# Kernel optimization log

Measured on AMD Instinct MI355X. Metric: run time of the kernel, lower is better.

## Reference

```python
import jax, jax.numpy as jnp
import numpy as np

B, L, D, NHEADS, P = 64, 256, 768, 8, 3
VOCAB, DEP, NLAYERS = 30522, 45, 2
LAM = 0.5


def _forward(src_mask, aspect_mask, lex, attention_mask,
             tok_emb, seg_emb, pool_w, pool_b, ln_a, ln_b,
             dep_emb, fc1_w, fc1_b, fc2_w, fc2_b,
             aq_w, aq_b, ak_w, ak_b, lq_w, lq_b, lk_w, lk_b, root_w,
             gcn_w, gcn_b, fc3_w, fc3_b, cls_w, cls_b, vlin_w,
             text_bert_indices, bert_segments_ids, ori_tag, head):
    b, l = text_bert_indices.shape
    d = tok_emb.shape[1]
    dk = d // NHEADS
    NEG = jnp.float32(-1e30)
    # stand-in BERT encoder: token + segment embeddings, tanh pooler on [CLS]
    seq = tok_emb[text_bert_indices] + seg_emb[bert_segments_ids]
    pooled = jnp.tanh(seq[:, 0] @ pool_w + pool_b)
    # torch LayerNorm variant: unbiased std (ddof=1)
    mean = seq.mean(-1, keepdims=True)
    std = jnp.std(seq, axis=-1, keepdims=True, ddof=1)
    gcn_in = ln_a * (seq - mean) / (std + 1e-6) + ln_b
    # in-place fmask[:,0]=1 mutates src_mask storage in torch -> effective mask
    sm = src_mask.at[:, 0].set(1.0)
    # dependency-tag score -> per-token softmax -> scatter into [L,L] adjacency
    dep_h = jax.nn.relu(dep_emb[ori_tag] @ fc1_w + fc1_b)
    dep_s = (dep_h @ fc2_w + fc2_b)[..., 0]                      # [B,L]
    dep_feat = jax.nn.softmax(dep_s * sm + (1.0 - sm) * NEG, axis=1)
    to_idx = jnp.arange(1, l)
    fro = head[:, :l - 1]                                        # [B,L-1]
    b_idx = jnp.arange(b)[:, None]
    vals = dep_feat[:, :l - 1]
    dep_adj = jnp.ones((b, l, l), jnp.float32)
    dep_adj = dep_adj.at[b_idx, fro, to_idx[None, :]].set(vals)
    dep_adj = dep_adj.at[b_idx, to_idx[None, :], fro].set(vals)
    # multi-head attention-as-adjacency (returns softmax weights only)
    q = (gcn_in @ aq_w + aq_b).reshape(b, l, NHEADS, dk).transpose(0, 2, 1, 3)
    k = (gcn_in @ ak_w + ak_b).reshape(b, l, NHEADS, dk).transpose(0, 2, 1, 3)
    scores = jnp.einsum('bhqd,bhkd->bhqk', q, k) / (jnp.sqrt(jnp.float32(dk)) + 1e-9)
    scores = jnp.where(sm[:, None, None, :] == 0, jnp.float32(-1e9), scores)
    adj_ag = jax.nn.softmax(scores, axis=-1).mean(axis=1)        # [B,L,L]
    eye = jnp.eye(l, dtype=jnp.float32)
    adj_ag = (adj_ag * (1.0 - eye) + eye) * sm[:, :, None]
    # structured latent attention (stand-in for missing StructuredAtt):
    # masked bilinear attention biased by dep_adj + root attention loss
    q2 = gcn_in @ lq_w + lq_b
    k2 = gcn_in @ lk_w + lk_b
    lat = jnp.einsum('bqd,bkd->bqk', q2, k2) / jnp.sqrt(jnp.float32(d))
    lat = lat + dep_adj + (1.0 - sm)[:, None, :] * (-10000.0)
    adj_latent = jax.nn.softmax(lat, axis=-1)
    root_p = jax.nn.softmax((gcn_in @ root_w)[..., 0] * sm + (1.0 - sm) * NEG, axis=1)
    loss_root = -jnp.mean(jnp.log(jnp.sum(root_p * aspect_mask, axis=1) + 1e-9))
    adj_latent = (adj_latent * (1.0 - eye) + eye) * sm[:, :, None]
    # gated dual-adjacency GCN layers
    H_l = gcn_in
    I_sem = gcn_in
    for layer in range(gcn_w.shape[0]):
        g_l = jax.nn.sigmoid(H_l)
        I_sem = (adj_ag @ H_l) @ gcn_w[layer] + gcn_b[layer]
        I_lat = (adj_latent @ H_l) @ gcn_w[layer] + gcn_b[layer]
        g = jax.nn.sigmoid(I_lat)
        lam_g = LAM * g
        I_com = (1.0 - lam_g) * I_sem + lam_g * I_lat
        H_out = jax.nn.relu(I_com @ fc3_w + fc3_b)
        H_l = g_l * H_out + (1.0 - g_l) * H_l
    # readout
    asp_wn = aspect_mask.sum(axis=1, keepdims=True)              # [B,1]
    m3 = sm[:, :, None]
    h_l = H_l * m3
    h_sem = I_sem * m3
    beta = jnp.einsum('bqd,bkd->bqk', h_l, h_sem) / 1000.0
    attn_o = jax.nn.softmax(beta.sum(axis=1, keepdims=True), axis=2)  # [B,1,L]
    outputs = (attn_o @ I_sem)[:, 0]                             # [B,D]
    sem_pool = (I_sem * aspect_mask[:, :, None]).sum(axis=1) / (asp_wn + 1e-9)
    final = jnp.concatenate([outputs, sem_pool, pooled], axis=-1)  # [B,3D]
    logits = final @ cls_w + cls_b
    e = (H_l @ vlin_w)[..., 0]
    lw = jax.nn.softmax(e, axis=1) * 50.0
    lw = lw * sm.at[:, 0].set(0.0)
    lexicon_loss = jnp.mean((lw - lex) ** 2)
    return logits, loss_root, lexicon_loss


def setup_inputs() -> dict:
    key = jax.random.key(0)
    ks = jax.random.split(key, 24)
    s = 0.02
    n = lambda i, shape: jax.random.normal(ks[i], shape, dtype=jnp.float32) * s
    inp = {}
    inp['text_bert_indices'] = jax.random.randint(ks[0], (B, L), 0, VOCAB, dtype=jnp.int32)
    inp['bert_segments_ids'] = jnp.zeros((B, L), jnp.int32)
    inp['attention_mask'] = jnp.ones((B, L), jnp.float32)
    inp['src_mask'] = jnp.ones((B, L), jnp.float32)
    inp['aspect_mask'] = jax.random.randint(ks[1], (B, L), 0, 2).astype(jnp.float32)
    inp['lex'] = jax.random.uniform(ks[2], (B, L), dtype=jnp.float32)
    inp['ori_tag'] = jax.random.randint(ks[3], (B, L), 0, DEP, dtype=jnp.int32)
    inp['head'] = jax.random.randint(ks[4], (B, L), 0, L, dtype=jnp.int32)
    inp['tok_emb'] = n(5, (VOCAB, D)); inp['seg_emb'] = n(6, (2, D))
    inp['pool_w'] = n(7, (D, D)); inp['pool_b'] = jnp.zeros((D,), jnp.float32)
    inp['ln_a'] = jnp.ones((D,), jnp.float32); inp['ln_b'] = jnp.zeros((D,), jnp.float32)
    inp['dep_emb'] = n(8, (DEP, 300))
    inp['fc1_w'] = n(9, (300, 256)); inp['fc1_b'] = jnp.zeros((256,), jnp.float32)
    inp['fc2_w'] = n(10, (256, 1)); inp['fc2_b'] = jnp.zeros((1,), jnp.float32)
    inp['aq_w'] = n(11, (D, D)); inp['aq_b'] = jnp.zeros((D,), jnp.float32)
    inp['ak_w'] = n(12, (D, D)); inp['ak_b'] = jnp.zeros((D,), jnp.float32)
    inp['lq_w'] = n(13, (D, D)); inp['lq_b'] = jnp.zeros((D,), jnp.float32)
    inp['lk_w'] = n(14, (D, D)); inp['lk_b'] = jnp.zeros((D,), jnp.float32)
    inp['root_w'] = n(15, (D, 1))
    inp['gcn_w'] = n(16, (NLAYERS, D, D)); inp['gcn_b'] = jnp.zeros((NLAYERS, D), jnp.float32)
    inp['fc3_w'] = n(17, (D, D)); inp['fc3_b'] = jnp.zeros((D,), jnp.float32)
    inp['cls_w'] = n(18, (3 * D, P)); inp['cls_b'] = jnp.zeros((P,), jnp.float32)
    inp['vlin_w'] = n(19, (D, 1))
    return inp


def reference(text_bert_indices, bert_segments_ids, attention_mask, src_mask, aspect_mask, lex,
              ori_tag, head, tok_emb, seg_emb, pool_w, pool_b, ln_a, ln_b, dep_emb,
              fc1_w, fc1_b, fc2_w, fc2_b, aq_w, aq_b, ak_w, ak_b, lq_w, lq_b, lk_w, lk_b,
              root_w, gcn_w, gcn_b, fc3_w, fc3_b, cls_w, cls_b, vlin_w):
    return _forward(src_mask, aspect_mask, lex, attention_mask,
                    tok_emb, seg_emb, pool_w, pool_b, ln_a, ln_b,
                    dep_emb, fc1_w, fc1_b, fc2_w, fc2_b,
                    aq_w, aq_b, ak_w, ak_b, lq_w, lq_b, lk_w, lk_b, root_w,
                    gcn_w, gcn_b, fc3_w, fc3_b, cls_w, cls_b, vlin_w,
                    text_bert_indices, bert_segments_ids, ori_tag, head)
```

## Files before the change

kernel.cpp:

```cpp
#include <hip/hip_runtime.h>
#include <hip/hip_bf16.h>
#include <math.h>

#define DI __device__ __forceinline__

constexpr int cB = 64, cL = 256, cD = 768;
constexpr long BLD = (long)cB * cL * cD;
constexpr long BLL = (long)cB * cL * cL;
constexpr long cLL = (long)cL * cL;
constexpr long cLD = (long)cL * cD;

typedef __attribute__((ext_vector_type(8))) short b8;
typedef __attribute__((ext_vector_type(4))) float f4;

#define GLDS(g, l)                                                    \
  __builtin_amdgcn_global_load_lds(                                   \
      (const __attribute__((address_space(1))) void*)(g),             \
      (__attribute__((address_space(3))) void*)(l), 16, 0, 0)

DI float wsum(float v) {
#pragma unroll
  for (int o = 32; o > 0; o >>= 1) v += __shfl_down(v, o, 64);
  return v;
}
DI float wsum_all(float v) {
#pragma unroll
  for (int m = 32; m > 0; m >>= 1) v += __shfl_xor(v, m, 64);
  return v;
}
DI float wmaxr(float v) {
#pragma unroll
  for (int o = 32; o > 0; o >>= 1) v = fmaxf(v, __shfl_down(v, o, 64));
  return v;
}
DI float blockSum(float v) {
  __shared__ float sh[4];
  v = wsum(v);
  __syncthreads();
  if ((threadIdx.x & 63) == 0) sh[threadIdx.x >> 6] = v;
  __syncthreads();
  return sh[0] + sh[1] + sh[2] + sh[3];
}
DI float blockMax(float v) {
  __shared__ float sh[4];
  v = wmaxr(v);
  __syncthreads();
  if ((threadIdx.x & 63) == 0) sh[threadIdx.x >> 6] = v;
  __syncthreads();
  return fmaxf(fmaxf(sh[0], sh[1]), fmaxf(sh[2], sh[3]));
}
DI float sigf(float x) { return 1.f / (1.f + expf(-x)); }

template <int OBF, int RELU, int BIAS, int EPI, int SWZ>
__global__ __launch_bounds__(256, 2) void bgemm(
    const __hip_bfloat16* __restrict__ A, const __hip_bfloat16* __restrict__ BT,
    void* __restrict__ Cv, const float* __restrict__ bias,
    float* __restrict__ auxf, __hip_bfloat16* __restrict__ auxb,
    int K, int lda, int ldb, int ldc,
    int zshift, int zmask, long sA1, long sA2, long sB1, long sB2, long sC,
    int czdiv) {
  __shared__ __hip_bfloat16 Asp[128 * 32];
  __shared__ __hip_bfloat16 Bsp[128 * 32];
  int bx = blockIdx.x, by = blockIdx.y;
  if (SWZ) {
    int gx = gridDim.x;
    int nb = gx * gridDim.y;
    int id = by * gx + bx;
    int cpx = nb >> 3;
    id = (id & 7) * cpx + (id >> 3);
    bx = id % gx;
    by = id / gx;
  }
  int z = blockIdx.z;
  A += (long)(z >> zshift) * sA1 + (long)(z & zmask) * sA2;
  BT += (long)(z >> zshift) * sB1 + (long)(z & zmask) * sB2;
  int tid = threadIdx.x;
  int lane = tid & 63, w = tid >> 6;
  int wr = w >> 1, wc = w & 1;
  int l16 = lane & 15, q = lane >> 4;
  int m0 = by << 7, n0 = bx << 7;

  int fm = tid >> 2, fq = tid & 3;
  const __hip_bfloat16* Ap0 = A + (long)(m0 + fm) * lda + fq * 8;
  const __hip_bfloat16* Ap1 = A + (long)(m0 + fm + 64) * lda + fq * 8;
  const __hip_bfloat16* Bp0 = BT + (long)(n0 + fm) * ldb + fq * 8;
  const __hip_bfloat16* Bp1 = BT + (long)(n0 + fm + 64) * ldb + fq * 8;
  char* Aw0 = (char*)Asp + (w << 10);
  char* Aw1 = (char*)Asp + 4096 + (w << 10);
  char* Bw0 = (char*)Bsp + (w << 10);
  char* Bw1 = (char*)Bsp + 4096 + (w << 10);

  f4 acc[4][4];
#pragma unroll
  for (int i = 0; i < 4; i++)
#pragma unroll
    for (int j = 0; j < 4; j++) acc[i][j] = (f4){0.f, 0.f, 0.f, 0.f};

  for (int k0 = 0; k0 < K; k0 += 32) {
    GLDS(Ap0 + k0, Aw0);
    GLDS(Ap1 + k0, Aw1);
    GLDS(Bp0 + k0, Bw0);
    GLDS(Bp1 + k0, Bw1);
    __syncthreads();
    b8 af[4], bf[4];
#pragma unroll
    for (int i = 0; i < 4; i++)
      af[i] = *(const b8*)&Asp[(wr * 64 + i * 16 + l16) * 32 + q * 8];
#pragma unroll
    for (int j = 0; j < 4; j++)
      bf[j] = *(const b8*)&Bsp[(wc * 64 + j * 16 + l16) * 32 + q * 8];
#pragma unroll
    for (int i = 0; i < 4; i++)
#pragma unroll
      for (int j = 0; j < 4; j++)
        acc[i][j] = __builtin_amdgcn_mfma_f32_16x16x32_bf16(af[i], bf[j], acc[i][j], 0, 0, 0);
    __syncthreads();
  }
  if (EPI == 4) {
#pragma unroll
    for (int j = 0; j < 4; j++) {
      int n = n0 + wc * 64 + j * 16 + l16;
#pragma unroll
      for (int i = 0; i < 4; i++) {
        int m = m0 + wr * 64 + i * 16 + (q << 2);
        __hip_bfloat16 t4[4];
#pragma unroll
        for (int r = 0; r < 4; r++) t4[r] = __float2bfloat16(acc[i][j][r]);
        long bidx = (long)(m >> 8) * sC + (long)n * cL + (m & 255);
        *(uint2*)&((__hip_bfloat16*)Cv)[bidx] = *(uint2*)t4;
      }
    }
    return;
  }
  long cz = (long)(z >> czdiv) * sC;
#pragma unroll
  for (int j = 0; j < 4; j++) {
    int n = n0 + wc * 64 + j * 16 + l16;
    float bv = BIAS ? bias[n] : 0.f;
#pragma unroll
    for (int i = 0; i < 4; i++) {
#pragma unroll
      for (int r = 0; r < 4; r++) {
        int m = m0 + wr * 64 + i * 16 + q * 4 + r;
        long idx = cz + (long)m * ldc + n;
        float v = acc[i][j][r] + bv;
        if (EPI == 0) {
          if (RELU) v = fmaxf(v, 0.f);
          if (OBF)
            ((__hip_bfloat16*)Cv)[idx] = __float2bfloat16(v);
          else
            ((float*)Cv)[idx] = v;
        } else {
          v = fmaxf(v, 0.f);
          float h = __bfloat162float(auxb[idx]);
          float g = sigf(h);
          float o = h + g * (v - h);
          auxb[idx] = __float2bfloat16(o);
          if (auxf) auxf[idx] = o;
        }
      }
    }
  }
}

__global__ __launch_bounds__(256, 2) void bgemm_dual(
    const __hip_bfloat16* __restrict__ A1g, const __hip_bfloat16* __restrict__ A2g,
    const __hip_bfloat16* __restrict__ BTg, float* __restrict__ IsemF,
    __hip_bfloat16* __restrict__ Icb, const float* __restrict__ bias,
    int write_isem) {
  __shared__ __hip_bfloat16 A1sp[128 * 32];
  __shared__ __hip_bfloat16 A2sp[128 * 32];
  __shared__ __hip_bfloat16 Bsp[128 * 32];
  int id = (blockIdx.z * 2 + blockIdx.y) * 6 + blockIdx.x;
  id = (id & 7) * 96 + (id >> 3);
  int bx = id % 6, t = id / 6;
  int by = t & 1, z = t >> 1;
  const __hip_bfloat16* A1 = A1g + (long)z * cLL;
  const __hip_bfloat16* A2 = A2g + (long)z * cLL;
  const __hip_bfloat16* BT = BTg + (long)z * cLD;
  int tid = threadIdx.x;
  int lane = tid & 63, w = tid >> 6;
  int wr = w >> 1, wc = w & 1;
  int l16 = lane & 15, q = lane >> 4;
  int m0 = by << 7, n0 = bx << 7;

  int fm = tid >> 2, fq = tid & 3;
  const __hip_bfloat16* A1p0 = A1 + (long)(m0 + fm) * cL + fq * 8;
  const __hip_bfloat16* A1p1 = A1p0 + 64L * cL;
  const __hip_bfloat16* A2p0 = A2 + (long)(m0 + fm) * cL + fq * 8;
  const __hip_bfloat16* A2p1 = A2p0 + 64L * cL;
  const __hip_bfloat16* Bp0 = BT + (long)(n0 + fm) * cL + fq * 8;
  const __hip_bfloat16* Bp1 = Bp0 + 64L * cL;
  char* w10 = (char*)A1sp + (w << 10);
  char* w11 = (char*)A1sp + 4096 + (w << 10);
  char* w20 = (char*)A2sp + (w << 10);
  char* w21 = (char*)A2sp + 4096 + (w << 10);
  char* wb0 = (char*)Bsp + (w << 10);
  char* wb1 = (char*)Bsp + 4096 + (w << 10);

  f4 ac1[4][4], ac2[4][4];
#pragma unroll
  for (int i = 0; i < 4; i++)
#pragma unroll
    for (int j = 0; j < 4; j++) {
      ac1[i][j] = (f4){0.f, 0.f, 0.f, 0.f};
      ac2[i][j] = (f4){0.f, 0.f, 0.f, 0.f};
    }

  for (int k0 = 0; k0 < cL; k0 += 32) {
    GLDS(A1p0 + k0, w10);
    GLDS(A1p1 + k0, w11);
    GLDS(A2p0 + k0, w20);
    GLDS(A2p1 + k0, w21);
    GLDS(Bp0 + k0, wb0);
    GLDS(Bp1 + k0, wb1);
    __syncthreads();
    b8 a1f[4], a2f[4], bf[4];
#pragma unroll
    for (int i = 0; i < 4; i++) {
      a1f[i] = *(const b8*)&A1sp[(wr * 64 + i * 16 + l16) * 32 + q * 8];
      a2f[i] = *(const b8*)&A2sp[(wr * 64 + i * 16 + l16) * 32 + q * 8];
    }
#pragma unroll
    for (int j = 0; j < 4; j++)
      bf[j] = *(const b8*)&Bsp[(wc * 64 + j * 16 + l16) * 32 + q * 8];
#pragma unroll
    for (int i = 0; i < 4; i++)
#pragma unroll
      for (int j = 0; j < 4; j++) {
        ac1[i][j] = __builtin_amdgcn_mfma_f32_16x16x32_bf16(a1f[i], bf[j], ac1[i][j], 0, 0, 0);
        ac2[i][j] = __builtin_amdgcn_mfma_f32_16x16x32_bf16(a2f[i], bf[j], ac2[i][j], 0, 0, 0);
      }
    __syncthreads();
  }
  long cz = (long)z * cLD;
#pragma unroll
  for (int j = 0; j < 4; j++) {
    int n = n0 + wc * 64 + j * 16 + l16;
    float bv = bias[n];
#pragma unroll
    for (int i = 0; i < 4; i++) {
#pragma unroll
      for (int r = 0; r < 4; r++) {
        int m = m0 + wr * 64 + i * 16 + q * 4 + r;
        long idx = cz + (long)m * cD + n;
        float is = ac1[i][j][r] + bv;
        float il = ac2[i][j][r] + bv;
        float g = 0.5f * sigf(il);
        Icb[idx] = __float2bfloat16(is + g * (il - is));
        if (write_isem) IsemF[idx] = is;
      }
    }
  }
}

__global__ __launch_bounds__(256, 2) void k_qkadj2(
    const __hip_bfloat16* __restrict__ qkb, const float* __restrict__ src_mask,
    const int* __restrict__ headv, const float* __restrict__ df,
    __hip_bfloat16* __restrict__ outAag, __hip_bfloat16* __restrict__ outAlat) {
  const bool lat = blockIdx.z != 0;
  const int NH = lat ? 1 : 8;
  const int KH = lat ? 768 : 96;
  const int QOFF = lat ? 1536 : 0;
  const int KOFF = lat ? 2304 : 768;
  const float scale = lat ? (1.f / sqrtf(768.f)) : (1.f / (sqrtf(96.f) + 1e-9f));
  __shared__ __hip_bfloat16 Qs[64 * 32];
  __shared__ __hip_bfloat16 Ks[256 * 32];
  __shared__ float red[4][64];
  const int b = blockIdx.y, m0 = blockIdx.x << 6;
  const int tid = threadIdx.x, lane = tid & 63, w = tid >> 6;
  const int l16 = lane & 15, q = lane >> 4;
  const long rowbase = (long)b * cL;
  const __hip_bfloat16* Qg = qkb + (rowbase + m0 + (tid >> 2)) * 3072 + (tid & 3) * 8 + QOFF;
  const __hip_bfloat16* Kg = qkb + (rowbase + (tid >> 2)) * 3072 + (tid & 3) * 8 + KOFF;
  char* qdst = (char*)Qs + (w << 10);

  float smj[4];
  int hcol[4];
  float dfc[4];
#pragma unroll
  for (int j = 0; j < 4; j++) {
    int col = w * 64 + j * 16 + l16;
    smj[j] = (col == 0) ? 1.f : src_mask[b * cL + col];
    if (lat) {
      hcol[j] = (col >= 1) ? headv[b * cL + col - 1] : -1;
      dfc[j] = (col >= 1) ? df[b * cL + col - 1] : 0.f;
    }
  }
  float smi_[4][4];
  int hrow_[4][4];
  float dfr_[4][4];
#pragma unroll
  for (int i = 0; i < 4; i++)
#pragma unroll
    for (int r = 0; r < 4; r++) {
      int grow = m0 + i * 16 + q * 4 + r;
      smi_[i][r] = (grow == 0) ? 1.f : src_mask[b * cL + grow];
      if (lat) {
        hrow_[i][r] = (grow >= 1) ? headv[b * cL + grow - 1] : -1;
        dfr_[i][r] = (grow >= 1) ? df[b * cL + grow - 1] : 0.f;
      }
    }

  f4 aag[4][4];
#pragma unroll
  for (int i = 0; i < 4; i++)
#pragma unroll
    for (int j = 0; j < 4; j++) aag[i][j] = (f4){0.f, 0.f, 0.f, 0.f};

  f4 sa[4][4];
  float inv_[4][4];
  for (int h = 0; h < NH; h++) {
    const int hk = h * 96;
#pragma unroll
    for (int i = 0; i < 4; i++)
#pragma unroll
      for (int j = 0; j < 4; j++) sa[i][j] = (f4){0.f, 0.f, 0.f, 0.f};
    for (int k0 = 0; k0 < KH; k0 += 32) {
      __syncthreads();
      GLDS(Qg + hk + k0, qdst);
#pragma unroll
      for (int u = 0; u < 4; u++)
        GLDS(Kg + (long)u * 196608 + hk + k0, (char*)Ks + u * 4096 + (w << 10));
      __syncthreads();
      b8 af[4], bf[4];
#pragma unroll
      for (int i = 0; i < 4; i++)
        af[i] = *(const b8*)&Qs[(i * 16 + l16) * 32 + q * 8];
#pragma unroll
      for (int j = 0; j < 4; j++)
        bf[j] = *(const b8*)&Ks[(w * 64 + j * 16 + l16) * 32 + q * 8];
#pragma unroll
      for (int i = 0; i < 4; i++)
#pragma unroll
        for (int j = 0; j < 4; j++)
          sa[i][j] = __builtin_amdgcn_mfma_f32_16x16x32_bf16(af[i], bf[j], sa[i][j], 0, 0, 0);
    }
#pragma unroll
    for (int i = 0; i < 4; i++)
#pragma unroll
      for (int j = 0; j < 4; j++)
#pragma unroll
        for (int r = 0; r < 4; r++) {
          float raw = sa[i][j][r];
          float v;
          if (lat) {
            int grow = m0 + i * 16 + q * 4 + r;
            int col = w * 64 + j * 16 + l16;
            float dep = 1.f;
            if (hcol[j] == grow) dep = dfc[j];
            if (col == hrow_[i][r]) dep = dfr_[i][r];
            v = raw * scale + dep + (1.f - smj[j]) * -10000.f;
          } else {
            v = (smj[j] == 0.f) ? -1e9f : raw * scale;
          }
          sa[i][j][r] = v;
        }
    float rm_[4][4];
#pragma unroll
    for (int i = 0; i < 4; i++)
#pragma unroll
      for (int r = 0; r < 4; r++) {
        float m = fmaxf(fmaxf(sa[i][0][r], sa[i][1][r]), fmaxf(sa[i][2][r], sa[i][3][r]));
#pragma unroll
        for (int o = 1; o < 16; o <<= 1) m = fmaxf(m, __shfl_xor(m, o, 64));
        if (l16 == 0) red[w][i * 16 + q * 4 + r] = m;
        rm_[i][r] = m;
      }
    __syncthreads();
#pragma unroll
    for (int i = 0; i < 4; i++)
#pragma unroll
      for (int r = 0; r < 4; r++) {
        int lr = i * 16 + q * 4 + r;
        rm_[i][r] = fmaxf(fmaxf(red[0][lr], red[1][lr]), fmaxf(red[2][lr], red[3][lr]));
      }
    __syncthreads();
#pragma unroll
    for (int i = 0; i < 4; i++)
#pragma unroll
      for (int r = 0; r < 4; r++) {
        float s0 = 0.f;
#pragma unroll
        for (int j = 0; j < 4; j++) {
          float e = expf(sa[i][j][r] - rm_[i][r]);
          sa[i][j][r] = e;
          s0 += e;
        }
#pragma unroll
        for (int o = 1; o < 16; o <<= 1) s0 += __shfl_xor(s0, o, 64);
        if (l16 == 0) red[w][i * 16 + q * 4 + r] = s0;
      }
    __syncthreads();
#pragma unroll
    for (int i = 0; i < 4; i++)
#pragma unroll
      for (int r = 0; r < 4; r++) {
        int lr = i * 16 + q * 4 + r;
        inv_[i][r] = 1.f / (red[0][lr] + red[1][lr] + red[2][lr] + red[3][lr]);
      }
    if (!lat) {
#pragma unroll
      for (int i = 0; i < 4; i++)
#pragma unroll
        for (int j = 0; j < 4; j++)
#pragma unroll
          for (int r = 0; r < 4; r++) aag[i][j][r] += sa[i][j][r] * inv_[i][r];
    }
  }
  __hip_bfloat16* outA = lat ? outAlat : outAag;
#pragma unroll
  for (int j = 0; j < 4; j++) {
    int col = w * 64 + j * 16 + l16;
#pragma unroll
    for (int i = 0; i < 4; i++)
#pragma unroll
      for (int r = 0; r < 4; r++) {
        int grow = m0 + i * 16 + q * 4 + r;
        float p = lat ? sa[i][j][r] * inv_[i][r] : aag[i][j][r] * 0.125f;
        float v = (col == grow) ? 1.f : p;
        outA[((long)b * cL + grow) * cL + col] = __float2bfloat16(v * smi_[i][r]);
      }
  }
}

__global__ void k_wconv7(const float* __restrict__ s0, const float* __restrict__ s1,
                         const float* __restrict__ s2, const float* __restrict__ s3,
                         const float* __restrict__ s4, const float* __restrict__ s5,
                         const float* __restrict__ s6, __hip_bfloat16* __restrict__ dst,
                         const float* __restrict__ ba, const float* __restrict__ bb,
                         const float* __restrict__ bc, const float* __restrict__ bd,
                         float* __restrict__ catb) {
  if (blockIdx.z == 7) {
    if (blockIdx.y != 0 || blockIdx.x >= 12) return;
    int tid = threadIdx.y * 32 + threadIdx.x;
    int i = blockIdx.x * 256 + tid;
    float v = (i < 768) ? ba[i] : (i < 1536) ? bb[i - 768]
              : (i < 2304) ? bc[i - 1536] : bd[i - 2304];
    catb[i] = v;
    return;
  }
  const float* srcs[7] = {s0, s1, s2, s3, s4, s5, s6};
  const float* src = srcs[blockIdx.z];
  __hip_bfloat16* d = dst + (long)blockIdx.z * cD * cD;
  __shared__ float t[32][33];
  int k0 = blockIdx.x * 32, n0 = blockIdx.y * 32;
  int tx = threadIdx.x, ty = threadIdx.y;
#pragma unroll
  for (int i = 0; i < 32; i += 8) t[ty + i][tx] = src[(long)(k0 + ty + i) * cD + n0 + tx];
  __syncthreads();
#pragma unroll
  for (int i = 0; i < 32; i += 8)
    d[(long)(n0 + ty + i) * cD + k0 + tx] = __float2bfloat16(t[tx][ty + i]);
}

__global__ __launch_bounds__(256) void k_gcnin(
    const int* __restrict__ tbi, const int* __restrict__ bsi,
    const float* __restrict__ tok, const float* __restrict__ seg,
    const float* __restrict__ ln_a, const float* __restrict__ ln_b,
    const float* __restrict__ root_w, __hip_bfloat16* __restrict__ gib,
    float* __restrict__ x64, float* __restrict__ e1) {
  int wave = threadIdx.x >> 6, lane = threadIdx.x & 63;
  long bl = (long)blockIdx.x * 4 + wave;
  int t = tbi[bl], s = bsi[bl];
  const float* tr = tok + (long)t * cD;
  const float* sr = seg + (long)s * cD;
  float x[12];
  float ls = 0.f;
#pragma unroll
  for (int c = 0; c < 12; c++) {
    int d = lane + (c << 6);
    x[c] = tr[d] + sr[d];
    ls += x[c];
  }
  if ((bl & 255) == 0) {
#pragma unroll
    for (int c = 0; c < 12; c++) x64[(bl >> 8) * cD + lane + (c << 6)] = x[c];
  }
  float mean = wsum_all(ls) * (1.f / 768.f);
  float lv = 0.f;
#pragma unroll
  for (int c = 0; c < 12; c++) { float d2 = x[c] - mean; lv += d2 * d2; }
  float var = wsum_all(lv) * (1.f / 767.f);
  float inv = 1.f / (sqrtf(var) + 1e-6f);
  float rdot = 0.f;
#pragma unroll
  for (int c = 0; c < 12; c++) {
    int d = lane + (c << 6);
    float v = ln_a[d] * (x[c] - mean) * inv + ln_b[d];
    gib[bl * cD + d] = __float2bfloat16(v);
    rdot += v * root_w[d];
  }
  float tot = wsum_all(rdot);
  if (lane == 0) e1[bl] = tot;
}

__global__ __launch_bounds__(256) void k_pool1(
    const float* __restrict__ x64, const float* __restrict__ pw,
    float* __restrict__ pacc) {
  __shared__ float pws[48][256];
  __shared__ float xs[16][48];
  int i0 = blockIdx.x * 48, j0 = blockIdx.y * 256, b0 = blockIdx.z * 16;
  for (int r = 0; r < 48; r++) pws[r][threadIdx.x] = pw[(long)(i0 + r) * cD + j0 + threadIdx.x];
  for (int idx = threadIdx.x; idx < 16 * 48; idx += 256)
    xs[idx / 48][idx % 48] = x64[(long)(b0 + idx / 48) * cD + i0 + idx % 48];
  __syncthreads();
  int j = threadIdx.x;
  for (int b = 0; b < 16; b++) {
    float acc = 0.f;
#pragma unroll 8
    for (int i = 0; i < 48; i++) acc += xs[b][i] * pws[i][j];
    atomicAdd(&pacc[(long)(b0 + b) * cD + j0 + j], acc);
  }
}

__global__ __launch_bounds__(256) void k_s45(
    const float* __restrict__ dep_emb, const float* __restrict__ fc1w,
    const float* __restrict__ fc1b, const float* __restrict__ fc2w,
    const float* __restrict__ fc2b, float* __restrict__ s45) {
  int t = blockIdx.x;
  __shared__ float e[300];
  for (int i = threadIdx.x; i < 300; i += 256) e[i] = dep_emb[t * 300 + i];
  __syncthreads();
  int j = threadIdx.x;
  float h = fc1b[j];
  for (int i = 0; i < 300; i++) h += e[i] * fc1w[i * 256 + j];
  h = fmaxf(h, 0.f);
  float tot = blockSum(h * fc2w[j]);
  if (threadIdx.x == 0) s45[t] = tot + fc2b[0];
}

__global__ __launch_bounds__(256) void k_depfeat(
    const int* __restrict__ ori, const float* __restrict__ src_mask,
    const float* __restrict__ s45, float* __restrict__ dep_feat) {
  int b = blockIdx.x, l = threadIdx.x;
  float smv = (l == 0) ? 1.f : src_mask[b * cL + l];
  float sc = s45[ori[b * cL + l]] * smv + (1.f - smv) * (-1e30f);
  float mx = blockMax(sc);
  float ex = expf(sc - mx);
  float sum = blockSum(ex);
  dep_feat[b * cL + l] = ex / sum;
}

__global__ __launch_bounds__(256) void k_rowdot2(
    const float* __restrict__ Isem, const float* __restrict__ hlsum,
    const float* __restrict__ gcnH, const float* __restrict__ vlin,
    float* __restrict__ sraw, float* __restrict__ e2) {
  int r = blockIdx.x * 4 + (threadIdx.x >> 6);
  int lane = threadIdx.x & 63;
  bool z = blockIdx.y != 0;
  const float4* row = (const float4*)((z ? gcnH : Isem) + (long)r * cD);
  const float4* wp = z ? (const float4*)vlin
                       : (const float4*)(hlsum + (long)(r >> 8) * cD);
  float s = 0.f;
#pragma unroll
  for (int c = 0; c < 3; c++) {
    int idx = c * 64 + lane;
    float4 a = row[idx], b = wp[idx];
    s += a.x * b.x + a.y * b.y + a.z * b.z + a.w * b.w;
  }
  s = wsum(s);
  if (lane == 0) (z ? e2 : sraw)[r] = s;
}

__global__ __launch_bounds__(256) void k_tailred(
    const float* __restrict__ sraw, const float* __restrict__ e1,
    const float* __restrict__ e2, const float* __restrict__ src_mask,
    const float* __restrict__ aspect_mask, const float* __restrict__ lex,
    float* __restrict__ wgt, float* __restrict__ asum,
    float* __restrict__ out_root, float* __restrict__ out_lex) {
  int b = blockIdx.x, l = threadIdx.x;
  float smv = (l == 0) ? 1.f : src_mask[b * cL + l];
  float am = aspect_mask[b * cL + l];
  float s = sraw[b * cL + l] * smv * 0.001f;
  float mx = blockMax(s);
  float ex = expf(s - mx);
  float sum = blockSum(ex);
  wgt[b * cL + l] = ex / sum;
  float a = blockSum(am);
  if (l == 0) asum[b] = a;
  float sc = e1[b * cL + l] * smv + (1.f - smv) * (-1e30f);
  float mx2 = blockMax(sc);
  float ex2 = expf(sc - mx2);
  float sum2 = blockSum(ex2);
  float tot = blockSum((ex2 / sum2) * am);
  if (l == 0) atomicAdd(out_root, -logf(tot + 1e-9f) * (1.f / 64.f));
  float e = e2[b * cL + l];
  float mx3 = blockMax(e);
  float ex3 = expf(e - mx3);
  float sum3 = blockSum(ex3);
  float mult = (l == 0) ? 0.f : src_mask[b * cL + l];
  float lw = ex3 / sum3 * 50.f * mult;
  float d2 = lw - lex[b * cL + l];
  float t3 = blockSum(d2 * d2);
  if (l == 0) atomicAdd(out_lex, t3 * (1.f / (64.f * 256.f)));
}

__global__ __launch_bounds__(256) void k_hl(
    const float* __restrict__ H, const float* __restrict__ src_mask,
    float* __restrict__ hlsum) {
  int b = blockIdx.z, d = (blockIdx.y << 8) + threadIdx.x, l0 = blockIdx.x * 32;
  float acc = 0.f;
  for (int l = l0; l < l0 + 32; l++) {
    float smv = (l == 0) ? 1.f : src_mask[b * cL + l];
    acc += H[((long)b * cL + l) * cD + d] * smv;
  }
  atomicAdd(&hlsum[(long)b * cD + d], acc);
}

__global__ __launch_bounds__(256) void k_wsum(
    const float* __restrict__ Isem, const float* __restrict__ wgt,
    const float* __restrict__ am, float* __restrict__ outputs,
    float* __restrict__ sempool) {
  int b = blockIdx.z, d = (blockIdx.y << 8) + threadIdx.x, l0 = blockIdx.x * 32;
  float accO = 0.f, accS = 0.f;
  for (int l = l0; l < l0 + 32; l++) {
    float v = Isem[((long)b * cL + l) * cD + d];
    accO += wgt[b * cL + l] * v;
    accS += am[b * cL + l] * v;
  }
  atomicAdd(&outputs[(long)b * cD + d], accO);
  atomicAdd(&sempool[(long)b * cD + d], accS);
}

__global__ __launch_bounds__(256) void k_logits(
    const float* __restrict__ outputs, const float* __restrict__ sempool,
    const float* __restrict__ pacc, const float* __restrict__ pb,
    const float* __restrict__ asum, const float* __restrict__ cw,
    const float* __restrict__ cb, float* __restrict__ out) {
  int b = blockIdx.x;
  float inv = 1.f / (asum[b] + 1e-9f);
  float a0 = 0.f, a1 = 0.f, a2 = 0.f;
  for (int i = threadIdx.x; i < 3 * cD; i += 256) {
    float f;
    if (i < cD)
      f = outputs[(long)b * cD + i];
    else if (i < 2 * cD)
      f = sempool[(long)b * cD + i - cD] * inv;
    else
      f = tanhf(pacc[(long)b * cD + i - 2 * cD] + pb[i - 2 * cD]);
    a0 += f * cw[i * 3 + 0];
    a1 += f * cw[i * 3 + 1];
    a2 += f * cw[i * 3 + 2];
  }
  a0 = blockSum(a0);
  a1 = blockSum(a1);
  a2 = blockSum(a2);
  if (threadIdx.x == 0) {
    out[b * 3 + 0] = a0 + cb[0];
    out[b * 3 + 1] = a1 + cb[1];
    out[b * 3 + 2] = a2 + cb[2];
  }
}

extern "C" void kernel_launch(void* const* d_in, const int* in_sizes, int n_in,
                              void* d_out, int out_size, void* d_ws, size_t ws_size,
                              hipStream_t stream) {
  const int* tbi = (const int*)d_in[0];
  const int* bsi = (const int*)d_in[1];
  const float* src_mask = (const float*)d_in[3];
  const float* aspect_mask = (const float*)d_in[4];
  const float* lex = (const float*)d_in[5];
  const int* ori = (const int*)d_in[6];
  const int* head = (const int*)d_in[7];
  const float* tok_emb = (const float*)d_in[8];
  const float* seg_emb = (const float*)d_in[9];
  const float* pool_w = (const float*)d_in[10];
  const float* pool_b = (const float*)d_in[11];
  const float* ln_a = (const float*)d_in[12];
  const float* ln_b = (const float*)d_in[13];
  const float* dep_emb = (const float*)d_in[14];
  const float* fc1_w = (const float*)d_in[15];
  const float* fc1_b = (const float*)d_in[16];
  const float* fc2_w = (const float*)d_in[17];
  const float* fc2_b = (const float*)d_in[18];
  const float* aq_w = (const float*)d_in[19];
  const float* aq_b = (const float*)d_in[20];
  const float* ak_w = (const float*)d_in[21];
  const float* ak_b = (const float*)d_in[22];
  const float* lq_w = (const float*)d_in[23];
  const float* lq_b = (const float*)d_in[24];
  const float* lk_w = (const float*)d_in[25];
  const float* lk_b = (const float*)d_in[26];
  const float* root_w = (const float*)d_in[27];
  const float* gcn_w = (const float*)d_in[28];
  const float* gcn_b = (const float*)d_in[29];
  const float* fc3_w = (const float*)d_in[30];
  const float* fc3_b = (const float*)d_in[31];
  const float* cls_w = (const float*)d_in[32];
  const float* cls_b = (const float*)d_in[33];
  const float* vlin_w = (const float*)d_in[34];

  float* out = (float*)d_out;
  float* ws = (float*)d_ws;
  float* gcnH = ws;
  float* Isem = gcnH + BLD;
  float* depfeat = Isem + BLD;
  float* s45 = depfeat + cB * cL;
  float* pooled = s45 + 64;
  float* x64 = pooled + cB * cD;
  float* hlsum = x64 + cB * cD;
  float* outputs = hlsum + cB * cD;
  float* sempool = outputs + cB * cD;
  float* pacc = sempool + cB * cD;
  float* e1 = pacc + cB * cD;
  float* e2 = e1 + cB * cL;
  float* sraw = e2 + cB * cL;
  float* wgt = sraw + cB * cL;
  float* asum = wgt + cB * cL;
  float* catb = asum + 64;
  __hip_bfloat16* gib = (__hip_bfloat16*)(catb + 3072);
  __hip_bfloat16* qkb = gib + BLD;
  __hip_bfloat16* scores = qkb + 4 * BLD;
  __hip_bfloat16* adjag_b = scores + 8 * BLL;
  __hip_bfloat16* adjlat_b = adjag_b + BLL;
  __hip_bfloat16* wbt = adjlat_b + BLL;
  __hip_bfloat16* HWbT = qkb + BLD;
  __hip_bfloat16* Icb = qkb + 2 * BLD;

  hipMemsetAsync((char*)d_out + 192 * sizeof(float), 0, 2 * sizeof(float), stream);
  hipMemsetAsync(hlsum, 0, 4 * cB * cD * sizeof(float), stream);

  k_gcnin<<<cB * cL / 4, 256, 0, stream>>>(tbi, bsi, tok_emb, seg_emb, ln_a, ln_b,
                                           root_w, gib, x64, e1);
  k_s45<<<45, 256, 0, stream>>>(dep_emb, fc1_w, fc1_b, fc2_w, fc2_b, s45);
  k_depfeat<<<cB, 256, 0, stream>>>(ori, src_mask, s45, depfeat);
  k_pool1<<<dim3(16, 3, 4), 256, 0, stream>>>(x64, pool_w, pacc);
  k_wconv7<<<dim3(24, 24, 8), dim3(32, 8), 0, stream>>>(
      aq_w, ak_w, lq_w, lk_w, gcn_w, gcn_w + (long)cD * cD, fc3_w, wbt,
      aq_b, ak_b, lq_b, lk_b, catb);

  const long DD = (long)cD * cD;
  const long LD = cLD;

  bgemm<1, 0, 1, 0, 1><<<dim3(24, 128, 1), 256, 0, stream>>>(
      gib, wbt, qkb, catb, nullptr, nullptr, cD, cD, cD, 3072,
      0, 0, 0, 0, 0, 0, 0, 0);

  k_qkadj2<<<dim3(4, cB, 2), 256, 0, stream>>>(qkb, src_mask, head, depfeat,
                                               adjag_b, adjlat_b);

  for (int layer = 0; layer < 2; layer++) {
    const float* bb = gcn_b + (long)layer * cD;
    bgemm<1, 0, 0, 4, 1><<<dim3(6, 128, 1), 256, 0, stream>>>(
        gib, wbt + (4 + layer) * DD, HWbT, nullptr, nullptr, nullptr,
        cD, cD, cD, cD, 0, 0, 0, 0, 0, 0, LD, 0);
    bgemm_dual<<<dim3(6, 2, cB), 256, 0, stream>>>(
        adjag_b, adjlat_b, HWbT, Isem, Icb, bb, layer == 1 ? 1 : 0);
    bgemm<0, 1, 1, 2, 1><<<dim3(6, 128, 1), 256, 0, stream>>>(
        Icb, wbt + 6 * DD, nullptr, fc3_b, layer == 1 ? gcnH : nullptr, gib,
        cD, cD, cD, cD, 0, 0, 0, 0, 0, 0, 0, 0);
  }

  k_hl<<<dim3(8, 3, cB), 256, 0, stream>>>(gcnH, src_mask, hlsum);
  k_rowdot2<<<dim3(cB * cL / 4, 2), 256, 0, stream>>>(Isem, hlsum, gcnH, vlin_w,
                                                      sraw, e2);
  k_tailred<<<cB, 256, 0, stream>>>(sraw, e1, e2, src_mask, aspect_mask, lex,
                                    wgt, asum, out + 192, out + 193);
  k_wsum<<<dim3(8, 3, cB), 256, 0, stream>>>(Isem, wgt, aspect_mask, outputs, sempool);
  k_logits<<<cB, 256, 0, stream>>>(outputs, sempool, pacc, pool_b, asum,
                                   cls_w, cls_b, out);
}
```

Before: 802.3 us.

## Restructure qkadj attention kernel so each wave owns full rows

Reworks the Q·K adjacency kernel so each wave computes 16 full rows across all 256 columns. This removes the cross-wave shared-memory max/sum reductions and their barriers. K is staged in 96-wide chunks into padded LDS (stride 104) and Q is read directly from global into registers. A swizzled block-id mapping interleaves the lat and ag workloads across blocks. The trade-off is much higher register use (16 accumulator tiles plus aag) and larger LDS, which may lower occupancy.

```diff
diff --git a/kernel.cpp b/kernel.cpp
--- a/kernel.cpp
+++ b/kernel.cpp
@@ -258,169 +258,170 @@
     const __hip_bfloat16* __restrict__ qkb, const float* __restrict__ src_mask,
     const int* __restrict__ headv, const float* __restrict__ df,
     __hip_bfloat16* __restrict__ outAag, __hip_bfloat16* __restrict__ outAlat) {
-  const bool lat = blockIdx.z != 0;
-  const int NH = lat ? 1 : 8;
-  const int KH = lat ? 768 : 96;
+  __shared__ __hip_bfloat16 Ks[256 * 104];
+  int id = (blockIdx.z * gridDim.y + blockIdx.y) * gridDim.x + blockIdx.x;
+  int W = (id & 7) * 64 + (id >> 3);
+  const bool lat = W >= 256;
+  int rem = W & 255;
+  const int b = rem >> 2, m0 = (rem & 3) << 6;
   const int QOFF = lat ? 1536 : 0;
   const int KOFF = lat ? 2304 : 768;
   const float scale = lat ? (1.f / sqrtf(768.f)) : (1.f / (sqrtf(96.f) + 1e-9f));
-  __shared__ __hip_bfloat16 Qs[64 * 32];
-  __shared__ __hip_bfloat16 Ks[256 * 32];
-  __shared__ float red[4][64];
-  const int b = blockIdx.y, m0 = blockIdx.x << 6;
   const int tid = threadIdx.x, lane = tid & 63, w = tid >> 6;
   const int l16 = lane & 15, q = lane >> 4;
   const long rowbase = (long)b * cL;
-  const __hip_bfloat16* Qg = qkb + (rowbase + m0 + (tid >> 2)) * 3072 + (tid & 3) * 8 + QOFF;
-  const __hip_bfloat16* Kg = qkb + (rowbase + (tid >> 2)) * 3072 + (tid & 3) * 8 + KOFF;
-  char* qdst = (char*)Qs + (w << 10);
-
-  float smj[4];
-  int hcol[4];
-  float dfc[4];
-#pragma unroll
-  for (int j = 0; j < 4; j++) {
-    int col = w * 64 + j * 16 + l16;
+  const __hip_bfloat16* Qbase =
+      qkb + (rowbase + m0 + w * 16 + l16) * 3072 + QOFF + q * 8;
+  const __hip_bfloat16* Kg = qkb + rowbase * 3072 + KOFF;
+  int kgo[13];
+#pragma unroll
+  for (int u = 0; u < 13; u++) {
+    int ci = u * 256 + tid;
+    int row = ci / 13, c16 = ci % 13;
+    if (c16 == 12) c16 = 0;
+    kgo[u] = row * 3072 + c16 * 8;
+  }
+  float smj[16];
+#pragma unroll
+  for (int j = 0; j < 16; j++) {
+    int col = j * 16 + l16;
     smj[j] = (col == 0) ? 1.f : src_mask[b * cL + col];
-    if (lat) {
+  }
+
+  f4 sa[16], aag[16];
+#pragma unroll
+  for (int j = 0; j < 16; j++) {
+    sa[j] = (f4){0.f, 0.f, 0.f, 0.f};
+    aag[j] = (f4){0.f, 0.f, 0.f, 0.f};
+  }
+
+  for (int c = 0; c < 8; c++) {
+    const int hk = c * 96;
+    if (c) __syncthreads();
+#pragma unroll
+    for (int u = 0; u < 13; u++)
+      GLDS(Kg + kgo[u] + hk, (char*)Ks + (u * 256 + w * 64) * 16);
+    __syncthreads();
+    if (!lat) {
+#pragma unroll
+      for (int j = 0; j < 16; j++) sa[j] = (f4){0.f, 0.f, 0.f, 0.f};
+    }
+#pragma unroll
+    for (int s = 0; s < 3; s++) {
+      b8 af = *(const b8*)(Qbase + hk + s * 32);
+#pragma unroll
+      for (int j = 0; j < 16; j++) {
+        b8 bf = *(const b8*)&Ks[(j * 16 + l16) * 104 + s * 32 + q * 8];
+        sa[j] = __builtin_amdgcn_mfma_f32_16x16x32_bf16(af, bf, sa[j], 0, 0, 0);
+      }
+    }
+    if (!lat) {
+      float rm[4] = {-1e30f, -1e30f, -1e30f, -1e30f};
+#pragma unroll
+      for (int j = 0; j < 16; j++)
+#pragma unroll
+        for (int r = 0; r < 4; r++) {
+          float v = (smj[j] == 0.f) ? -1e9f : sa[j][r] * scale;
+          sa[j][r] = v;
+          rm[r] = fmaxf(rm[r], v);
+        }
+#pragma unroll
+      for (int r = 0; r < 4; r++)
+#pragma unroll
+        for (int o = 1; o < 16; o <<= 1) rm[r] = fmaxf(rm[r], __shfl_xor(rm[r], o, 64));
+      float sum[4] = {0.f, 0.f, 0.f, 0.f};
+#pragma unroll
+      for (int j = 0; j < 16; j++)
+#pragma unroll
+        for (int r = 0; r < 4; r++) {
+          float e = expf(sa[j][r] - rm[r]);
+          sa[j][r] = e;
+          sum[r] += e;
+        }
+#pragma unroll
+      for (int r = 0; r < 4; r++) {
+#pragma unroll
+        for (int o = 1; o < 16; o <<= 1) sum[r] += __shfl_xor(sum[r], o, 64);
+        sum[r] = 1.f / sum[r];
+      }
+#pragma unroll
+      for (int j = 0; j < 16; j++)
+#pragma unroll
+        for (int r = 0; r < 4; r++) aag[j][r] += sa[j][r] * sum[r];
+    }
+  }
+
+  float inv[4];
+  if (lat) {
+    int hcol[16];
+    float dfc[16];
+#pragma unroll
+    for (int j = 0; j < 16; j++) {
+      int col = j * 16 + l16;
       hcol[j] = (col >= 1) ? headv[b * cL + col - 1] : -1;
       dfc[j] = (col >= 1) ? df[b * cL + col - 1] : 0.f;
     }
-  }
-  float smi_[4][4];
-  int hrow_[4][4];
-  float dfr_[4][4];
-#pragma unroll
-  for (int i = 0; i < 4; i++)
+    int hrow_[4];
+    float dfr_[4];
 #pragma unroll
     for (int r = 0; r < 4; r++) {
-      int grow = m0 + i * 16 + q * 4 + r;
-      smi_[i][r] = (grow == 0) ? 1.f : src_mask[b * cL + grow];
-      if (lat) {
-        hrow_[i][r] = (grow >= 1) ? headv[b * cL + grow - 1] : -1;
-        dfr_[i][r] = (grow >= 1) ? df[b * cL + grow - 1] : 0.f;
+      int grow = m0 + w * 16 + q * 4 + r;
+      hrow_[r] = (grow >= 1) ? headv[b * cL + grow - 1] : -1;
+      dfr_[r] = (grow >= 1) ? df[b * cL + grow - 1] : 0.f;
+    }
+    float rm[4] = {-1e30f, -1e30f, -1e30f, -1e30f};
+#pragma unroll
+    for (int j = 0; j < 16; j++) {
+      int col = j * 16 + l16;
+#pragma unroll
+      for (int r = 0; r < 4; r++) {
+        int grow = m0 + w * 16 + q * 4 + r;
+        float dep = 1.f;
+        if (hcol[j] == grow) dep = dfc[j];
+        if (col == hrow_[r]) dep = dfr_[r];
+        float v = sa[j][r] * scale + dep + (1.f - smj[j]) * -10000.f;
+        sa[j][r] = v;
+        rm[r] = fmaxf(rm[r], v);
       }
     }
-
-  f4 aag[4][4];
-#pragma unroll
-  for (int i = 0; i < 4; i++)
-#pragma unroll
-    for (int j = 0; j < 4; j++) aag[i][j] = (f4){0.f, 0.f, 0.f, 0.f};
-
-  f4 sa[4][4];
-  float inv_[4][4];
-  for (int h = 0; h < NH; h++) {
-    const int hk = h * 96;
-#pragma unroll
-    for (int i = 0; i < 4; i++)
-#pragma unroll
-      for (int j = 0; j < 4; j++) sa[i][j] = (f4){0.f, 0.f, 0.f, 0.f};
-    for (int k0 = 0; k0 < KH; k0 += 32) {
-      __syncthreads();
-      GLDS(Qg + hk + k0, qdst);
-#pragma unroll
-      for (int u = 0; u < 4; u++)
-        GLDS(Kg + (long)u * 196608 + hk + k0, (char*)Ks + u * 4096 + (w << 10));
-      __syncthreads();
-      b8 af[4], bf[4];
-#pragma unroll
-      for (int i = 0; i < 4; i++)
-        af[i] = *(const b8*)&Qs[(i * 16 + l16) * 32 + q * 8];
-#pragma unroll
-      for (int j = 0; j < 4; j++)
-        bf[j] = *(const b8*)&Ks[(w * 64 + j * 16 + l16) * 32 + q * 8];
-#pragma unroll
-      for (int i = 0; i < 4; i++)
-#pragma unroll
-        for (int j = 0; j < 4; j++)
-          sa[i][j] = __builtin_amdgcn_mfma_f32_16x16x32_bf16(af[i], bf[j], sa[i][j], 0, 0, 0);
-    }
-#pragma unroll
-    for (int i = 0; i < 4; i++)
-#pragma unroll
-      for (int j = 0; j < 4; j++)
-#pragma unroll
-        for (int r = 0; r < 4; r++) {
-          float raw = sa[i][j][r];
-          float v;
-          if (lat) {
-            int grow = m0 + i * 16 + q * 4 + r;
-            int col = w * 64 + j * 16 + l16;
-            float dep = 1.f;
-            if (hcol[j] == grow) dep = dfc[j];
-            if (col == hrow_[i][r]) dep = dfr_[i][r];
-            v = raw * scale + dep + (1.f - smj[j]) * -10000.f;
-          } else {
-            v = (smj[j] == 0.f) ? -1e9f : raw * scale;
-          }
-          sa[i][j][r] = v;
-        }
-    float rm_[4][4];
-#pragma unroll
-    for (int i = 0; i < 4; i++)
+#pragma unroll
+    for (int r = 0; r < 4; r++)
+#pragma unroll
+      for (int o = 1; o < 16; o <<= 1) rm[r] = fmaxf(rm[r], __shfl_xor(rm[r], o, 64));
+    float sum[4] = {0.f, 0.f, 0.f, 0.f};
+#pragma unroll
+    for (int j = 0; j < 16; j++)
 #pragma unroll
       for (int r = 0; r < 4; r++) {
-        float m = fmaxf(fmaxf(sa[i][0][r], sa[i][1][r]), fmaxf(sa[i][2][r], sa[i][3][r]));
-#pragma unroll
-        for (int o = 1; o < 16; o <<= 1) m = fmaxf(m, __shfl_xor(m, o, 64));
-        if (l16 == 0) red[w][i * 16 + q * 4 + r] = m;
-        rm_[i][r] = m;
+        float e = expf(sa[j][r] - rm[r]);
+        sa[j][r] = e;
+        sum[r] += e;
       }
-    __syncthreads();
-#pragma unroll
-    for (int i = 0; i < 4; i++)
-#pragma unroll
-      for (int r = 0; r < 4; r++) {
-        int lr = i * 16 + q * 4 + r;
-        rm_[i][r] = fmaxf(fmaxf(red[0][lr], red[1][lr]), fmaxf(red[2][lr], red[3][lr]));
-      }
-    __syncthreads();
-#pragma unroll
-    for (int i = 0; i < 4; i++)
-#pragma unroll
-      for (int r = 0; r < 4; r++) {
-        float s0 = 0.f;
-#pragma unroll
-        for (int j = 0; j < 4; j++) {
-          float e = expf(sa[i][j][r] - rm_[i][r]);
-          sa[i][j][r] = e;
-          s0 += e;
-        }
-#pragma unroll
-        for (int o = 1; o < 16; o <<= 1) s0 += __shfl_xor(s0, o, 64);
-        if (l16 == 0) red[w][i * 16 + q * 4 + r] = s0;
-      }
-    __syncthreads();
-#pragma unroll
-    for (int i = 0; i < 4; i++)
-#pragma unroll
-      for (int r = 0; r < 4; r++) {
-        int lr = i * 16 + q * 4 + r;
-        inv_[i][r] = 1.f / (red[0][lr] + red[1][lr] + red[2][lr] + red[3][lr]);
-      }
-    if (!lat) {
-#pragma unroll
-      for (int i = 0; i < 4; i++)
-#pragma unroll
-        for (int j = 0; j < 4; j++)
-#pragma unroll
-          for (int r = 0; r < 4; r++) aag[i][j][r] += sa[i][j][r] * inv_[i][r];
-    }
+#pragma unroll
+    for (int r = 0; r < 4; r++) {
+#pragma unroll
+      for (int o = 1; o < 16; o <<= 1) sum[r] += __shfl_xor(sum[r], o, 64);
+      inv[r] = 1.f / sum[r];
+    }
+  }
+
+  float smi_[4];
+#pragma unroll
+  for (int r = 0; r < 4; r++) {
+    int grow = m0 + w * 16 + q * 4 + r;
+    smi_[r] = (grow == 0) ? 1.f : src_mask[b * cL + grow];
   }
   __hip_bfloat16* outA = lat ? outAlat : outAag;
 #pragma unroll
-  for (int j = 0; j < 4; j++) {
-    int col = w * 64 + j * 16 + l16;
-#pragma unroll
-    for (int i = 0; i < 4; i++)
-#pragma unroll
-      for (int r = 0; r < 4; r++) {
-        int grow = m0 + i * 16 + q * 4 + r;
-        float p = lat ? sa[i][j][r] * inv_[i][r] : aag[i][j][r] * 0.125f;
-        float v = (col == grow) ? 1.f : p;
-        outA[((long)b * cL + grow) * cL + col] = __float2bfloat16(v * smi_[i][r]);
-      }
+  for (int j = 0; j < 16; j++) {
+    int col = j * 16 + l16;
+#pragma unroll
+    for (int r = 0; r < 4; r++) {
+      int grow = m0 + w * 16 + q * 4 + r;
+      float p = lat ? sa[j][r] * inv[r] : aag[j][r] * 0.125f;
+      float v = (col == grow) ? 1.f : p;
+      outA[((long)b * cL + grow) * cL + col] = __float2bfloat16(v * smi_[r]);
+    }
   }
 }
 
```

Result: slower. 841.4 us (+4.9%).

## Double-buffer Q/K tiles in qkadj kernel with flattened head loop and block remap

Applied to the files above, without the earlier changes.

Rewrites the attention-adjacency kernel's main loop as a single 24-step K loop with double-buffered LDS tiles. The next tile's async global-to-LDS loads overlap the MFMA work, gated by vmcnt waits and raw s_barrier calls instead of two __syncthreads per step. The per-head softmax for the multi-head path is folded in every third step. Block IDs are remapped so ag and lat blocks interleave across the grid, and mask/head loads are deferred to after the loop to ease register pressure. This doubles LDS use, which may reduce occupancy, and relies on hand-written waitcnt counts being correct.

```diff
diff --git a/kernel.cpp b/kernel.cpp
--- a/kernel.cpp
+++ b/kernel.cpp
@@ -17,6 +17,15 @@
   __builtin_amdgcn_global_load_lds(                                   \
       (const __attribute__((address_space(1))) void*)(g),             \
       (__attribute__((address_space(3))) void*)(l), 16, 0, 0)
+
+#define SCB __builtin_amdgcn_sched_barrier(0)
+DI void rbar() { SCB; __builtin_amdgcn_s_barrier(); SCB; }
+DI void lbar() {
+  asm volatile("s_waitcnt lgkmcnt(0)" ::: "memory");
+  SCB;
+  __builtin_amdgcn_s_barrier();
+  SCB;
+}
 
 DI float wsum(float v) {
 #pragma unroll
@@ -258,104 +267,168 @@
     const __hip_bfloat16* __restrict__ qkb, const float* __restrict__ src_mask,
     const int* __restrict__ headv, const float* __restrict__ df,
     __hip_bfloat16* __restrict__ outAag, __hip_bfloat16* __restrict__ outAlat) {
-  const bool lat = blockIdx.z != 0;
-  const int NH = lat ? 1 : 8;
-  const int KH = lat ? 768 : 96;
+  __shared__ __hip_bfloat16 Qs[2][64 * 32];
+  __shared__ __hip_bfloat16 Ks[2][256 * 32];
+  __shared__ float red[4][64];
+  int id = (blockIdx.z * gridDim.y + blockIdx.y) * gridDim.x + blockIdx.x;
+  int W = (id & 7) * 64 + (id >> 3);
+  const bool lat = W >= 256;
+  int rem = W & 255;
+  const int b = rem >> 2, m0 = (rem & 3) << 6;
   const int QOFF = lat ? 1536 : 0;
   const int KOFF = lat ? 2304 : 768;
   const float scale = lat ? (1.f / sqrtf(768.f)) : (1.f / (sqrtf(96.f) + 1e-9f));
-  __shared__ __hip_bfloat16 Qs[64 * 32];
-  __shared__ __hip_bfloat16 Ks[256 * 32];
-  __shared__ float red[4][64];
-  const int b = blockIdx.y, m0 = blockIdx.x << 6;
   const int tid = threadIdx.x, lane = tid & 63, w = tid >> 6;
   const int l16 = lane & 15, q = lane >> 4;
   const long rowbase = (long)b * cL;
-  const __hip_bfloat16* Qg = qkb + (rowbase + m0 + (tid >> 2)) * 3072 + (tid & 3) * 8 + QOFF;
-  const __hip_bfloat16* Kg = qkb + (rowbase + (tid >> 2)) * 3072 + (tid & 3) * 8 + KOFF;
-  char* qdst = (char*)Qs + (w << 10);
+  const __hip_bfloat16* Qg =
+      qkb + (rowbase + m0 + (tid >> 2)) * 3072 + (tid & 3) * 8 + QOFF;
+  const __hip_bfloat16* Kg =
+      qkb + (rowbase + (tid >> 2)) * 3072 + (tid & 3) * 8 + KOFF;
 
   float smj[4];
-  int hcol[4];
-  float dfc[4];
 #pragma unroll
   for (int j = 0; j < 4; j++) {
     int col = w * 64 + j * 16 + l16;
     smj[j] = (col == 0) ? 1.f : src_mask[b * cL + col];
-    if (lat) {
+  }
+
+  f4 sa[4][4], aag[4][4];
+#pragma unroll
+  for (int i = 0; i < 4; i++)
+#pragma unroll
+    for (int j = 0; j < 4; j++) {
+      sa[i][j] = (f4){0.f, 0.f, 0.f, 0.f};
+      aag[i][j] = (f4){0.f, 0.f, 0.f, 0.f};
+    }
+
+  auto STAGE = [&](int s, int p) {
+    GLDS(Qg + s * 32, (char*)Qs[p] + (w << 10));
+#pragma unroll
+    for (int u = 0; u < 4; u++)
+      GLDS(Kg + (long)u * 196608 + s * 32, (char*)Ks[p] + u * 4096 + (w << 10));
+  };
+
+  STAGE(0, 0);
+  STAGE(1, 1);
+
+  for (int s = 0; s < 24; s++) {
+    const int p = s & 1;
+    if (s < 23) {
+      asm volatile("s_waitcnt vmcnt(5)" ::: "memory");
+    } else {
+      asm volatile("s_waitcnt vmcnt(0)" ::: "memory");
+    }
+    rbar();
+    if (!lat && (s % 3) == 0) {
+#pragma unroll
+      for (int i = 0; i < 4; i++)
+#pragma unroll
+        for (int j = 0; j < 4; j++) sa[i][j] = (f4){0.f, 0.f, 0.f, 0.f};
+    }
+    b8 af[4], bf[4];
+#pragma unroll
+    for (int i = 0; i < 4; i++)
+      af[i] = *(const b8*)&Qs[p][(i * 16 + l16) * 32 + q * 8];
+#pragma unroll
+    for (int j = 0; j < 4; j++)
+      bf[j] = *(const b8*)&Ks[p][(w * 64 + j * 16 + l16) * 32 + q * 8];
+#pragma unroll
+    for (int i = 0; i < 4; i++)
+#pragma unroll
+      for (int j = 0; j < 4; j++)
+        sa[i][j] = __builtin_amdgcn_mfma_f32_16x16x32_bf16(af[i], bf[j], sa[i][j], 0, 0, 0);
+    rbar();
+    if (s + 2 < 24) STAGE(s + 2, p);
+    if (!lat && (s % 3) == 2) {
+#pragma unroll
+      for (int i = 0; i < 4; i++)
+#pragma unroll
+        for (int j = 0; j < 4; j++)
+#pragma unroll
+          for (int r = 0; r < 4; r++)
+            sa[i][j][r] = (smj[j] == 0.f) ? -1e9f : sa[i][j][r] * scale;
+      float rm_[4][4];
+#pragma unroll
+      for (int i = 0; i < 4; i++)
+#pragma unroll
+        for (int r = 0; r < 4; r++) {
+          float m = fmaxf(fmaxf(sa[i][0][r], sa[i][1][r]), fmaxf(sa[i][2][r], sa[i][3][r]));
+#pragma unroll
+          for (int o = 1; o < 16; o <<= 1) m = fmaxf(m, __shfl_xor(m, o, 64));
+          if (l16 == 0) red[w][i * 16 + q * 4 + r] = m;
+        }
+      lbar();
+#pragma unroll
+      for (int i = 0; i < 4; i++)
+#pragma unroll
+        for (int r = 0; r < 4; r++) {
+          int lr = i * 16 + q * 4 + r;
+          rm_[i][r] = fmaxf(fmaxf(red[0][lr], red[1][lr]), fmaxf(red[2][lr], red[3][lr]));
+        }
+      lbar();
+#pragma unroll
+      for (int i = 0; i < 4; i++)
+#pragma unroll
+        for (int r = 0; r < 4; r++) {
+          float s0 = 0.f;
+#pragma unroll
+          for (int j = 0; j < 4; j++) {
+            float e = expf(sa[i][j][r] - rm_[i][r]);
+            sa[i][j][r] = e;
+            s0 += e;
+          }
+#pragma unroll
+          for (int o = 1; o < 16; o <<= 1) s0 += __shfl_xor(s0, o, 64);
+          if (l16 == 0) red[w][i * 16 + q * 4 + r] = s0;
+        }
+      lbar();
+#pragma unroll
+      for (int i = 0; i < 4; i++)
+#pragma unroll
+        for (int r = 0; r < 4; r++) {
+          int lr = i * 16 + q * 4 + r;
+          float iv = 1.f / (red[0][lr] + red[1][lr] + red[2][lr] + red[3][lr]);
+#pragma unroll
+          for (int j = 0; j < 4; j++) aag[i][j][r] += sa[i][j][r] * iv;
+        }
+    }
+  }
+
+  float inv_[4][4];
+  if (lat) {
+    int hcol[4];
+    float dfc[4];
+#pragma unroll
+    for (int j = 0; j < 4; j++) {
+      int col = w * 64 + j * 16 + l16;
       hcol[j] = (col >= 1) ? headv[b * cL + col - 1] : -1;
       dfc[j] = (col >= 1) ? df[b * cL + col - 1] : 0.f;
     }
-  }
-  float smi_[4][4];
-  int hrow_[4][4];
-  float dfr_[4][4];
-#pragma unroll
-  for (int i = 0; i < 4; i++)
-#pragma unroll
-    for (int r = 0; r < 4; r++) {
-      int grow = m0 + i * 16 + q * 4 + r;
-      smi_[i][r] = (grow == 0) ? 1.f : src_mask[b * cL + grow];
-      if (lat) {
+    int hrow_[4][4];
+    float dfr_[4][4];
+#pragma unroll
+    for (int i = 0; i < 4; i++)
+#pragma unroll
+      for (int r = 0; r < 4; r++) {
+        int grow = m0 + i * 16 + q * 4 + r;
         hrow_[i][r] = (grow >= 1) ? headv[b * cL + grow - 1] : -1;
         dfr_[i][r] = (grow >= 1) ? df[b * cL + grow - 1] : 0.f;
       }
-    }
-
-  f4 aag[4][4];
-#pragma unroll
-  for (int i = 0; i < 4; i++)
-#pragma unroll
-    for (int j = 0; j < 4; j++) aag[i][j] = (f4){0.f, 0.f, 0.f, 0.f};
-
-  f4 sa[4][4];
-  float inv_[4][4];
-  for (int h = 0; h < NH; h++) {
-    const int hk = h * 96;
-#pragma unroll
-    for (int i = 0; i < 4; i++)
-#pragma unroll
-      for (int j = 0; j < 4; j++) sa[i][j] = (f4){0.f, 0.f, 0.f, 0.f};
-    for (int k0 = 0; k0 < KH; k0 += 32) {
-      __syncthreads();
-      GLDS(Qg + hk + k0, qdst);
-#pragma unroll
-      for (int u = 0; u < 4; u++)
-        GLDS(Kg + (long)u * 196608 + hk + k0, (char*)Ks + u * 4096 + (w << 10));
-      __syncthreads();
-      b8 af[4], bf[4];
-#pragma unroll
-      for (int i = 0; i < 4; i++)
-        af[i] = *(const b8*)&Qs[(i * 16 + l16) * 32 + q * 8];
-#pragma unroll
-      for (int j = 0; j < 4; j++)
-        bf[j] = *(const b8*)&Ks[(w * 64 + j * 16 + l16) * 32 + q * 8];
-#pragma unroll
-      for (int i = 0; i < 4; i++)
-#pragma unroll
-        for (int j = 0; j < 4; j++)
-          sa[i][j] = __builtin_amdgcn_mfma_f32_16x16x32_bf16(af[i], bf[j], sa[i][j], 0, 0, 0);
-    }
-#pragma unroll
-    for (int i = 0; i < 4; i++)
-#pragma unroll
-      for (int j = 0; j < 4; j++)
+#pragma unroll
+    for (int i = 0; i < 4; i++)
+#pragma unroll
+      for (int j = 0; j < 4; j++) {
+        int col = w * 64 + j * 16 + l16;
 #pragma unroll
         for (int r = 0; r < 4; r++) {
-          float raw = sa[i][j][r];
-          float v;
-          if (lat) {
-            int grow = m0 + i * 16 + q * 4 + r;
-            int col = w * 64 + j * 16 + l16;
-            float dep = 1.f;
-            if (hcol[j] == grow) dep = dfc[j];
-            if (col == hrow_[i][r]) dep = dfr_[i][r];
-            v = raw * scale + dep + (1.f - smj[j]) * -10000.f;
-          } else {
-            v = (smj[j] == 0.f) ? -1e9f : raw * scale;
-          }
-          sa[i][j][r] = v;
+          int grow = m0 + i * 16 + q * 4 + r;
+          float dep = 1.f;
+          if (hcol[j] == grow) dep = dfc[j];
+          if (col == hrow_[i][r]) dep = dfr_[i][r];
+          sa[i][j][r] = sa[i][j][r] * scale + dep + (1.f - smj[j]) * -10000.f;
         }
+      }
     float rm_[4][4];
 #pragma unroll
     for (int i = 0; i < 4; i++)
@@ -365,9 +438,8 @@
 #pragma unroll
         for (int o = 1; o < 16; o <<= 1) m = fmaxf(m, __shfl_xor(m, o, 64));
         if (l16 == 0) red[w][i * 16 + q * 4 + r] = m;
-        rm_[i][r] = m;
-      }
-    __syncthreads();
+      }
+    lbar();
 #pragma unroll
     for (int i = 0; i < 4; i++)
 #pragma unroll
@@ -375,7 +447,7 @@
         int lr = i * 16 + q * 4 + r;
         rm_[i][r] = fmaxf(fmaxf(red[0][lr], red[1][lr]), fmaxf(red[2][lr], red[3][lr]));
       }
-    __syncthreads();
+    lbar();
 #pragma unroll
     for (int i = 0; i < 4; i++)
 #pragma unroll
@@ -391,7 +463,7 @@
         for (int o = 1; o < 16; o <<= 1) s0 += __shfl_xor(s0, o, 64);
         if (l16 == 0) red[w][i * 16 + q * 4 + r] = s0;
       }
-    __syncthreads();
+    lbar();
 #pragma unroll
     for (int i = 0; i < 4; i++)
 #pragma unroll
@@ -399,15 +471,16 @@
         int lr = i * 16 + q * 4 + r;
         inv_[i][r] = 1.f / (red[0][lr] + red[1][lr] + red[2][lr] + red[3][lr]);
       }
-    if (!lat) {
-#pragma unroll
-      for (int i = 0; i < 4; i++)
-#pragma unroll
-        for (int j = 0; j < 4; j++)
-#pragma unroll
-          for (int r = 0; r < 4; r++) aag[i][j][r] += sa[i][j][r] * inv_[i][r];
-    }
-  }
+  }
+
+  float smi_[4][4];
+#pragma unroll
+  for (int i = 0; i < 4; i++)
+#pragma unroll
+    for (int r = 0; r < 4; r++) {
+      int grow = m0 + i * 16 + q * 4 + r;
+      smi_[i][r] = (grow == 0) ? 1.f : src_mask[b * cL + grow];
+    }
   __hip_bfloat16* outA = lat ? outAlat : outAag;
 #pragma unroll
   for (int j = 0; j < 4; j++) {
```

Result: faster. 727.6 us (-9.3%).
